# Kernel optimization log

Hardware: AMD Instinct MI355X
Metric: run time of the kernel (lower is better)

## Reference

```python
import jax, jax.numpy as jnp
import numpy as np

BITS = 8

def _quantize(w, bits=BITS):
    # Symmetric per-tensor quantization: round to (2^(bits-1)-1) levels, dequantize.
    n = float(2 ** (bits - 1) - 1)
    scale = jnp.max(jnp.abs(w)) / n
    wq = jnp.clip(jnp.round(w / scale), -n, n) * scale
    return wq

def setup_inputs() -> dict:
    key = jax.random.key(0)
    k1, k2, k3 = jax.random.split(key, 3)
    B, S, IN, OUT = 4, 2048, 4096, 4096
    x = jax.random.normal(k1, (B, S, IN), dtype=jnp.float32)
    weight = jax.random.normal(k2, (OUT, IN), dtype=jnp.float32)
    bias = jax.random.normal(k3, (OUT,), dtype=jnp.float32)
    return {"x": x, "weight": weight, "bias": bias}

def reference(x, weight, bias):
    # Original expand+cumsum trick is mathematically y = x @ quant(w).T + bias.
    wq = _quantize(weight)                      # (OUT, IN)
    y = jnp.einsum('bsi,oi->bso', x, wq)        # (B, S, OUT)
    return y + bias
```

## Files before the change

kernel.cpp:

```cpp
#include <hip/hip_runtime.h>
#include <hip/hip_bf16.h>
#include <stdint.h>


using short8  = __attribute__((ext_vector_type(8))) short;
using float4v = __attribute__((ext_vector_type(4))) float;


__device__ __forceinline__ unsigned short f2bf(float f) {
    union { float f; uint32_t u; } v; v.f = f;
    uint32_t u = v.u;
    u += 0x7fffu + ((u >> 16) & 1u);
    return (unsigned short)(u >> 16);
}

__device__ __forceinline__ void gload_lds16(const unsigned short* g, unsigned short* l) {
    __builtin_amdgcn_global_load_lds(
        (const __attribute__((address_space(1))) void*)g,
        (__attribute__((address_space(3))) void*)l,
        16, 0, 0);
}


__global__ void absmax_kernel(const float* __restrict__ w, int n4, unsigned int* __restrict__ out) {
    const float4* w4 = (const float4*)w;
    float m = 0.f;
    for (int i = blockIdx.x * blockDim.x + threadIdx.x; i < n4; i += gridDim.x * blockDim.x) {
        float4 v = w4[i];
        m = fmaxf(m, fmaxf(fmaxf(fabsf(v.x), fabsf(v.y)), fmaxf(fabsf(v.z), fabsf(v.w))));
    }
    #pragma unroll
    for (int off = 32; off > 0; off >>= 1)
        m = fmaxf(m, __shfl_down(m, off, 64));
    __shared__ float smax[8];
    int lane = threadIdx.x & 63, wv = threadIdx.x >> 6;
    if (lane == 0) smax[wv] = m;
    __syncthreads();
    if (threadIdx.x == 0) {
        float bm = smax[0];
        for (int i = 1; i < (int)(blockDim.x >> 6); i++) bm = fmaxf(bm, smax[i]);
        atomicMax(out, __float_as_uint(bm));
    }
}

__global__ void quant_kernel(const float* __restrict__ w, int n4,
                             const unsigned int* __restrict__ amax_bits,
                             ushort4* __restrict__ wq) {
    const float amax  = __uint_as_float(*amax_bits);
    const float scale = amax / 127.0f;
    const float inv   = 1.0f / scale;
    const float4* w4 = (const float4*)w;
    for (int i = blockIdx.x * blockDim.x + threadIdx.x; i < n4; i += gridDim.x * blockDim.x) {
        float4 v = w4[i];
        float q0 = fminf(fmaxf(rintf(v.x * inv), -127.f), 127.f);
        float q1 = fminf(fmaxf(rintf(v.y * inv), -127.f), 127.f);
        float q2 = fminf(fmaxf(rintf(v.z * inv), -127.f), 127.f);
        float q3 = fminf(fmaxf(rintf(v.w * inv), -127.f), 127.f);
        ushort4 o;
        o.x = f2bf(q0 * scale); o.y = f2bf(q1 * scale);
        o.z = f2bf(q2 * scale); o.w = f2bf(q3 * scale);
        wq[i] = o;
    }
}

__global__ void cvt_bf16_kernel(const float4* __restrict__ in, ushort4* __restrict__ out, int n4) {
    for (int i = blockIdx.x * blockDim.x + threadIdx.x; i < n4; i += gridDim.x * blockDim.x) {
        float4 v = in[i];
        ushort4 o;
        o.x = f2bf(v.x); o.y = f2bf(v.y); o.z = f2bf(v.z); o.w = f2bf(v.w);
        out[i] = o;
    }
}


__global__ __launch_bounds__(256) void gemm_bt(
    const unsigned short* __restrict__ A,
    const unsigned short* __restrict__ B,
    const float* __restrict__ bias,
    float* __restrict__ C,
    int M, int N, int K)
{
    __shared__ __align__(16) unsigned short As[128 * 32];
    __shared__ __align__(16) unsigned short Bs[128 * 32];

    const int tid  = threadIdx.x;
    const int lane = tid & 63;
    const int wave = tid >> 6;
    const int wm   = wave >> 1;
    const int wn   = wave & 1;

    const int bm = blockIdx.y * 128;
    const int bn = blockIdx.x * 128;

    const int srow = wave * 32 + (lane >> 2);
    const int skc  = (lane & 3) * 8;

    const unsigned short* Ag0 = A + (size_t)(bm + srow) * K + skc;
    const unsigned short* Ag1 = Ag0 + (size_t)16 * K;
    const unsigned short* Bg0 = B + (size_t)(bn + srow) * K + skc;
    const unsigned short* Bg1 = Bg0 + (size_t)16 * K;

    unsigned short* sA0 = As + wave * 1024;
    unsigned short* sA1 = sA0 + 512;
    unsigned short* sB0 = Bs + wave * 1024;
    unsigned short* sB1 = sB0 + 512;

    const int frow = lane & 15;
    const int fkc  = (lane >> 4) * 8;
    const unsigned short* pa = As + (wm * 64 + frow) * 32 + fkc;
    const unsigned short* pb = Bs + (wn * 64 + frow) * 32 + fkc;

    float4v acc[4][4];
    const float4v zero = {0.f, 0.f, 0.f, 0.f};
    #pragma unroll
    for (int i = 0; i < 4; i++)
        #pragma unroll
        for (int j = 0; j < 4; j++) acc[i][j] = zero;

    for (int k0 = 0; k0 < K; k0 += 32) {
        gload_lds16(Ag0, sA0);
        gload_lds16(Ag1, sA1);
        gload_lds16(Bg0, sB0);
        gload_lds16(Bg1, sB1);
        Ag0 += 32; Ag1 += 32; Bg0 += 32; Bg1 += 32;
        __syncthreads();

        short8 a[4], b[4];
        #pragma unroll
        for (int i = 0; i < 4; i++) a[i] = *(const short8*)(pa + i * (16 * 32));
        #pragma unroll
        for (int j = 0; j < 4; j++) b[j] = *(const short8*)(pb + j * (16 * 32));

        #pragma unroll
        for (int i = 0; i < 4; i++)
            #pragma unroll
            for (int j = 0; j < 4; j++)
                acc[i][j] = __builtin_amdgcn_mfma_f32_16x16x32_bf16(a[i], b[j], acc[i][j], 0, 0, 0);

        __syncthreads();
    }

    const int quad = lane >> 4;
    const int cl   = lane & 15;
    #pragma unroll
    for (int j = 0; j < 4; j++) {
        const int gc = bn + wn * 64 + j * 16 + cl;
        const float bs = bias[gc];
        #pragma unroll
        for (int i = 0; i < 4; i++) {
            const int gr = bm + wm * 64 + i * 16 + quad * 4;
            float* cp = C + (size_t)gr * N + gc;
            #pragma unroll
            for (int r = 0; r < 4; r++)
                cp[(size_t)r * N] = acc[i][j][r] + bs;
        }
    }
}


extern "C" void kernel_launch(void* const* d_in, const int* in_sizes, int n_in,
                              void* d_out, int out_size, void* d_ws, size_t ws_size,
                              hipStream_t stream) {
    const float* x    = (const float*)d_in[0];
    const float* w    = (const float*)d_in[1];
    const float* bias = (const float*)d_in[2];
    float* out = (float*)d_out;

    const int M = 8192, N = 4096, K = 4096;

    const size_t wq_off   = 256;
    const size_t wq_bytes = (size_t)N * K * 2;
    unsigned int*   amax = (unsigned int*)d_ws;
    unsigned short* wq   = (unsigned short*)((char*)d_ws + wq_off);
    unsigned short* xb   = (unsigned short*)((char*)d_ws + wq_off + wq_bytes);

    size_t avail = (ws_size > wq_off + wq_bytes) ? ws_size - wq_off - wq_bytes : 0;
    int nch = 1;
    while (nch < 64 && (size_t)(M / nch) * K * 2 > avail) nch <<= 1;
    const int crows = M / nch;

    hipMemsetAsync(d_ws, 0, 256, stream);
    absmax_kernel<<<1024, 256, 0, stream>>>(w, (N * K) / 4, amax);
    quant_kernel<<<1024, 256, 0, stream>>>(w, (N * K) / 4, amax, (ushort4*)wq);

    for (int c = 0; c < nch; c++) {
        const float* xc = x + (size_t)c * crows * K;
        cvt_bf16_kernel<<<1024, 256, 0, stream>>>((const float4*)xc, (ushort4*)xb,
                                                  (crows * K) / 4);
        dim3 grid(N / 128, crows / 128);
        gemm_bt<<<grid, 256, 0, stream>>>(xb, wq, bias, out + (size_t)c * crows * N,
                                          crows, N, K);
    }
}
```

Baseline: 631.7 us.

## Swizzle GEMM LDS tiles and fuse absmax with activation bf16 conversion

Applies an XOR-like rotation to the 16-byte k-chunk position of each row in LDS, on both the global→LDS stores and the MFMA fragment reads, to cut LDS bank conflicts on the short8 fragment loads. It also merges the weight absmax reduction and the x fp32→bf16 conversion into one launch that splits its blocks between the two jobs, removing a separate kernel. M is now taken from the input size. In the chunked fallback path only half the launched blocks do the conversion, so part of x would be left unconverted if that path ever ran.

```diff
diff --git a/kernel.cpp b/kernel.cpp
--- a/kernel.cpp
+++ b/kernel.cpp
@@ -22,26 +22,40 @@
 }
 
 
-__global__ void absmax_kernel(const float* __restrict__ w, int n4, unsigned int* __restrict__ out) {
-    const float4* w4 = (const float4*)w;
-    float m = 0.f;
-    for (int i = blockIdx.x * blockDim.x + threadIdx.x; i < n4; i += gridDim.x * blockDim.x) {
-        float4 v = w4[i];
-        m = fmaxf(m, fmaxf(fmaxf(fabsf(v.x), fabsf(v.y)), fmaxf(fabsf(v.z), fabsf(v.w))));
-    }
-    #pragma unroll
-    for (int off = 32; off > 0; off >>= 1)
-        m = fmaxf(m, __shfl_down(m, off, 64));
-    __shared__ float smax[8];
-    int lane = threadIdx.x & 63, wv = threadIdx.x >> 6;
-    if (lane == 0) smax[wv] = m;
-    __syncthreads();
-    if (threadIdx.x == 0) {
-        float bm = smax[0];
-        for (int i = 1; i < (int)(blockDim.x >> 6); i++) bm = fmaxf(bm, smax[i]);
-        atomicMax(out, __float_as_uint(bm));
-    }
-}
+#define AB 1024
+#define CB 2048
+
+__global__ void prep_kernel(const float* __restrict__ w, int wn4,
+                            const float4* __restrict__ x, ushort4* __restrict__ xb, int xn4,
+                            unsigned int* __restrict__ amax_out) {
+    if (blockIdx.x < AB) {
+        const float4* w4 = (const float4*)w;
+        float m = 0.f;
+        for (int i = blockIdx.x * blockDim.x + threadIdx.x; i < wn4; i += AB * blockDim.x) {
+            float4 v = w4[i];
+            m = fmaxf(m, fmaxf(fmaxf(fabsf(v.x), fabsf(v.y)), fmaxf(fabsf(v.z), fabsf(v.w))));
+        }
+        #pragma unroll
+        for (int off = 32; off > 0; off >>= 1)
+            m = fmaxf(m, __shfl_down(m, off, 64));
+        __shared__ float smax[4];
+        int lane = threadIdx.x & 63, wv = threadIdx.x >> 6;
+        if (lane == 0) smax[wv] = m;
+        __syncthreads();
+        if (threadIdx.x == 0) {
+            float bm = fmaxf(fmaxf(smax[0], smax[1]), fmaxf(smax[2], smax[3]));
+            atomicMax(amax_out, __float_as_uint(bm));
+        }
+    } else {
+        for (int i = (blockIdx.x - AB) * blockDim.x + threadIdx.x; i < xn4; i += CB * blockDim.x) {
+            float4 v = x[i];
+            ushort4 o;
+            o.x = f2bf(v.x); o.y = f2bf(v.y); o.z = f2bf(v.z); o.w = f2bf(v.w);
+            xb[i] = o;
+        }
+    }
+}
+
 
 __global__ void quant_kernel(const float* __restrict__ w, int n4,
                              const unsigned int* __restrict__ amax_bits,
@@ -63,15 +77,6 @@
     }
 }
 
-__global__ void cvt_bf16_kernel(const float4* __restrict__ in, ushort4* __restrict__ out, int n4) {
-    for (int i = blockIdx.x * blockDim.x + threadIdx.x; i < n4; i += gridDim.x * blockDim.x) {
-        float4 v = in[i];
-        ushort4 o;
-        o.x = f2bf(v.x); o.y = f2bf(v.y); o.z = f2bf(v.z); o.w = f2bf(v.w);
-        out[i] = o;
-    }
-}
-
 
 __global__ __launch_bounds__(256) void gemm_bt(
     const unsigned short* __restrict__ A,
@@ -93,7 +98,7 @@
     const int bn = blockIdx.x * 128;
 
     const int srow = wave * 32 + (lane >> 2);
-    const int skc  = (lane & 3) * 8;
+    const int skc  = (((lane & 3) - (lane >> 3)) & 3) * 8;
 
     const unsigned short* Ag0 = A + (size_t)(bm + srow) * K + skc;
     const unsigned short* Ag1 = Ag0 + (size_t)16 * K;
@@ -106,9 +111,10 @@
     unsigned short* sB1 = sB0 + 512;
 
     const int frow = lane & 15;
-    const int fkc  = (lane >> 4) * 8;
-    const unsigned short* pa = As + (wm * 64 + frow) * 32 + fkc;
-    const unsigned short* pb = Bs + (wn * 64 + frow) * 32 + fkc;
+    const int fc   = lane >> 4;
+    const int poff = (frow * 4 + ((fc + (frow >> 1)) & 3)) * 8;
+    const unsigned short* pa = As + wm * 64 * 32 + poff;
+    const unsigned short* pb = Bs + wn * 64 * 32 + poff;
 
     float4v acc[4][4];
     const float4v zero = {0.f, 0.f, 0.f, 0.f};
@@ -127,9 +133,9 @@
 
         short8 a[4], b[4];
         #pragma unroll
-        for (int i = 0; i < 4; i++) a[i] = *(const short8*)(pa + i * (16 * 32));
-        #pragma unroll
-        for (int j = 0; j < 4; j++) b[j] = *(const short8*)(pb + j * (16 * 32));
+        for (int i = 0; i < 4; i++) a[i] = *(const short8*)(pa + i * 512);
+        #pragma unroll
+        for (int j = 0; j < 4; j++) b[j] = *(const short8*)(pb + j * 512);
 
         #pragma unroll
         for (int i = 0; i < 4; i++)
@@ -166,7 +172,8 @@
     const float* bias = (const float*)d_in[2];
     float* out = (float*)d_out;
 
-    const int M = 8192, N = 4096, K = 4096;
+    const int N = 4096, K = 4096;
+    const int M = in_sizes[0] / K;
 
     const size_t wq_off   = 256;
     const size_t wq_bytes = (size_t)N * K * 2;
@@ -180,15 +187,25 @@
     const int crows = M / nch;
 
     hipMemsetAsync(d_ws, 0, 256, stream);
-    absmax_kernel<<<1024, 256, 0, stream>>>(w, (N * K) / 4, amax);
-    quant_kernel<<<1024, 256, 0, stream>>>(w, (N * K) / 4, amax, (ushort4*)wq);
-
-    for (int c = 0; c < nch; c++) {
-        const float* xc = x + (size_t)c * crows * K;
-        cvt_bf16_kernel<<<1024, 256, 0, stream>>>((const float4*)xc, (ushort4*)xb,
-                                                  (crows * K) / 4);
-        dim3 grid(N / 128, crows / 128);
-        gemm_bt<<<grid, 256, 0, stream>>>(xb, wq, bias, out + (size_t)c * crows * N,
-                                          crows, N, K);
-    }
-}
+
+    if (nch == 1) {
+        prep_kernel<<<AB + CB, 256, 0, stream>>>(w, (N * K) / 4,
+                                                 (const float4*)x, (ushort4*)xb, (M * K) / 4,
+                                                 amax);
+        quant_kernel<<<2048, 256, 0, stream>>>(w, (N * K) / 4, amax, (ushort4*)wq);
+        dim3 grid(N / 128, M / 128);
+        gemm_bt<<<grid, 256, 0, stream>>>(xb, wq, bias, out, M, N, K);
+    } else {
+        prep_kernel<<<AB, 256, 0, stream>>>(w, (N * K) / 4,
+                                            (const float4*)x, (ushort4*)xb, 0, amax);
+        quant_kernel<<<2048, 256, 0, stream>>>(w, (N * K) / 4, amax, (ushort4*)wq);
+        for (int c = 0; c < nch; c++) {
+            const float* xc = x + (size_t)c * crows * K;
+            prep_kernel<<<CB, 256, 0, stream>>>(nullptr, 0, (const float4*)xc, (ushort4*)xb,
+                                                (crows * K) / 4, amax);
+            dim3 grid(N / 128, crows / 128);
+            gemm_bt<<<grid, 256, 0, stream>>>(xb, wq, bias, out + (size_t)c * crows * N,
+                                              crows, N, K);
+        }
+    }
+}
```

Result: no change. 628.5 us (-0.5%).
